# Performance work log

Hardware: AMD Instinct MI355X
Metric: run time of the kernel (lower is better)

The kernel has to match this reference:

```python
import jax, jax.numpy as jnp
import numpy as np

G = 128            # fine grid side -> N0 = 16384 nodes
C = 128            # hidden channels
CL = 4             # voxel cluster side (scale = CL/G = 1/32)
GC = G // CL       # coarse grid side = 32
NC = GC * GC       # 1024 coarse nodes
L = 6              # 3 MP blocks (down0, down1, up0) x 2 MP layers each


def _build_graph():
    ii, jj = np.meshgrid(np.arange(G), np.arange(G), indexing='ij')
    nid = ii * G + jj
    s_h, t_h = nid[:, :-1].ravel(), nid[:, 1:].ravel()
    s_v, t_v = nid[:-1, :].ravel(), nid[1:, :].ravel()
    src = np.concatenate([s_h, t_h, s_v, t_v]).astype(np.int64)
    dst = np.concatenate([t_h, s_h, t_v, s_v]).astype(np.int64)
    # voxel_grid(pos, size=1/32) on the unit square -> cluster id per node
    perm = ((ii // CL) * GC + (jj // CL)).ravel().astype(np.int64)
    ms, mt = perm[src], perm[dst]
    key = ms * NC + mt
    nonself = ms != mt
    uk = np.unique(key[nonself])                  # pool_edge: remove self loops + coalesce (sorted)
    E1 = int(uk.shape[0])
    e2c = np.where(nonself, np.searchsorted(uk, key), E1).astype(np.int64)
    pooled_ei = np.stack([uk // NC, uk % NC]).astype(np.int64)
    # unpool_edge: first fine edge whose mapped endpoints match each coarse edge
    first = np.full(E1 + 1, src.shape[0], dtype=np.int64)
    np.minimum.at(first, e2c, np.arange(src.shape[0], dtype=np.int64))
    perm_edges = first[:E1]
    return np.stack([src, dst]), perm, pooled_ei, e2c, perm_edges


def setup_inputs() -> dict:
    key = jax.random.key(0)
    ks = jax.random.split(key, 10)
    ei, perm, pei, e2c, pe = _build_graph()
    N0, E0 = G * G, ei.shape[1]
    s = 0.05
    return {
        'x': jax.random.normal(ks[0], (N0, C), jnp.float32),
        'edge_attr': jax.random.normal(ks[1], (E0, C), jnp.float32),
        'We1': jax.random.normal(ks[2], (L, 3 * C, C), jnp.float32) * s,
        'be1': jax.random.normal(ks[3], (L, C), jnp.float32) * s,
        'We2': jax.random.normal(ks[4], (L, C, C), jnp.float32) * s,
        'be2': jax.random.normal(ks[5], (L, C), jnp.float32) * s,
        'Wn1': jax.random.normal(ks[6], (L, 2 * C, C), jnp.float32) * s,
        'bn1': jax.random.normal(ks[7], (L, C), jnp.float32) * s,
        'Wn2': jax.random.normal(ks[8], (L, C, C), jnp.float32) * s,
        'bn2': jax.random.normal(ks[9], (L, C), jnp.float32) * s,
        'edge_index': jnp.asarray(ei),
        'perm': jnp.asarray(perm),
        'pooled_edge_index': jnp.asarray(pei),
        'edge_to_coarse': jnp.asarray(e2c),
        'perm_edges': jnp.asarray(pe),
    }


def _mp_block(x, e, src, dst, n, layers, We1, be1, We2, be2, Wn1, bn1, Wn2, bn2):
    # Residual message-passing block: edge MLP on [e, x_src, x_dst], node MLP on [x, sum_msg]
    for l in layers:
        m = jnp.concatenate([e, x[src], x[dst]], axis=-1)          # [E, 3C]
        e = e + (jax.nn.relu(m @ We1[l] + be1[l]) @ We2[l] + be2[l])
        agg = jax.ops.segment_sum(e, dst, num_segments=n)          # [N, C]
        h = jnp.concatenate([x, agg], axis=-1)                     # [N, 2C]
        x = x + (jax.nn.relu(h @ Wn1[l] + bn1[l]) @ Wn2[l] + bn2[l])
    return x, e


def reference(x, edge_attr, We1, be1, We2, be2, Wn1, bn1, Wn2, bn2,
              edge_index, perm, pooled_edge_index, edge_to_coarse, perm_edges):
    p = (We1, be1, We2, be2, Wn1, bn1, Wn2, bn2)
    N0 = x.shape[0]
    src0, dst0 = edge_index[0], edge_index[1]
    # down conv 0 (fine level)
    x0, e0 = _mp_block(x, edge_attr, src0, dst0, N0, (0, 1), *p)
    # avg_pool: mean node features per cluster, coalesce-sum edge attrs
    counts = jax.ops.segment_sum(jnp.ones((N0, 1), x.dtype), perm, num_segments=NC)
    x1 = jax.ops.segment_sum(x0, perm, num_segments=NC) / counts
    E1 = pooled_edge_index.shape[1]
    ea1 = jax.ops.segment_sum(e0, edge_to_coarse, num_segments=E1 + 1)[:E1]
    # down conv 1 (coarse level)
    x1, ea1 = _mp_block(x1, ea1, pooled_edge_index[0], pooled_edge_index[1], NC, (2, 3), *p)
    # unpool + sum-res skip connections
    xu = x0 + x1[perm]
    eu = e0 + jnp.zeros_like(e0).at[perm_edges].set(ea1)
    # up conv
    return _mp_block(xu, eu, src0, dst0, N0, (4, 5), *p)
```

## Files before the change

kernel.cpp:

```cpp
#include <hip/hip_runtime.h>

#define C_ 128
#define N0 16384
#define E0 65024
#define NC_ 1024
#define E1C 3968
#define LSTR 40
#define HSTR 36

typedef __attribute__((ext_vector_type(8))) short bf16x8;
typedef __attribute__((ext_vector_type(16))) float f32x16;

#define OFF_WE1 0
#define OFF_WE2 294912
#define OFF_WN1 393216
#define OFF_WN2 589824
#define W_TOTAL 688128

__device__ __forceinline__ void bsplit(float a, unsigned short& hi, unsigned short& lo) {
  unsigned ab = __float_as_uint(a);
  unsigned hb = ab & 0xFFFF0000u;
  hi = (unsigned short)(hb >> 16);
  float r = a - __uint_as_float(hb);
  lo = (unsigned short)(__float_as_uint(r) >> 16);
}

__device__ __forceinline__ int cprefix(int ci, int cj) {
  int rows = (ci == 0) ? 0 : (94 + (ci - 1) * 126);
  int v = (ci > 0) + (ci < 31);
  int within = (cj == 0) ? 0 : (2 * cj - 1);
  return rows + within + cj * v;
}

__device__ __forceinline__ void add4(float4& s, const float* p) {
  float4 v = *(const float4*)p;
  s.x += v.x; s.y += v.y; s.z += v.z; s.w += v.w;
}

__device__ __forceinline__ f32x16 zero16() {
  f32x16 z;
  #pragma unroll
  for (int i = 0; i < 16; ++i) z[i] = 0.f;
  return z;
}

__global__ void prep_weights(const float* __restrict__ We1, const float* __restrict__ We2,
                             const float* __restrict__ Wn1, const float* __restrict__ Wn2,
                             short* __restrict__ wh, short* __restrict__ wl) {
  int idx = blockIdx.x * 256 + threadIdx.x;
  const float* src; int Kt, off, rem;
  if (idx < 294912)      { src = We1; Kt = 384; off = OFF_WE1; rem = idx; }
  else if (idx < 393216) { src = We2; Kt = 128; off = OFF_WE2; rem = idx - 294912; }
  else if (idx < 589824) { src = Wn1; Kt = 256; off = OFF_WN1; rem = idx - 393216; }
  else                   { src = Wn2; Kt = 128; off = OFF_WN2; rem = idx - 589824; }
  int per_layer = Kt << 7;
  int layer = rem / per_layer;
  int r2 = rem - layer * per_layer;
  int k = r2 >> 7;
  int col = r2 & 127;
  float a = src[layer * per_layer + (k << 7) + col];
  unsigned short hi, lo;
  bsplit(a, hi, lo);
  int dst = off + layer * ((Kt >> 5) << 12) + ((k >> 5) << 12) + (col << 5) + (k & 31);
  wh[dst] = (short)hi;
  wl[dst] = (short)lo;
}

__device__ __forceinline__ void stage_w(short* sWh, short* sWl,
                                        const short* __restrict__ Wh,
                                        const short* __restrict__ Wl,
                                        int kc, int tid) {
  const short* srcH = Wh + (kc << 12);
  const short* srcL = Wl + (kc << 12);
  #pragma unroll
  for (int u0 = 0; u0 < 2; ++u0) {
    int u = tid + u0 * 256;
    int col = u >> 2, part = u & 3;
    *(uint4*)&sWh[col * LSTR + part * 8] = *(const uint4*)(srcH + u * 8);
    *(uint4*)&sWl[col * LSTR + part * 8] = *(const uint4*)(srcL + u * 8);
  }
}

#define BSPLIT8(V0, V1, AH, AL) do { \
    unsigned short h0_,h1_,h2_,h3_,h4_,h5_,h6_,h7_, l0_,l1_,l2_,l3_,l4_,l5_,l6_,l7_; \
    bsplit((V0).x,h0_,l0_); bsplit((V0).y,h1_,l1_); bsplit((V0).z,h2_,l2_); bsplit((V0).w,h3_,l3_); \
    bsplit((V1).x,h4_,l4_); bsplit((V1).y,h5_,l5_); bsplit((V1).z,h6_,l6_); bsplit((V1).w,h7_,l7_); \
    AH = (bf16x8){(short)h0_,(short)h1_,(short)h2_,(short)h3_,(short)h4_,(short)h5_,(short)h6_,(short)h7_}; \
    AL = (bf16x8){(short)l0_,(short)l1_,(short)l2_,(short)l3_,(short)l4_,(short)l5_,(short)l6_,(short)l7_}; \
  } while (0)

#define MFMA3(ACC, AH, AL, BH, BL) do { \
    ACC = __builtin_amdgcn_mfma_f32_32x32x16_bf16(AH, BH, ACC, 0, 0, 0); \
    ACC = __builtin_amdgcn_mfma_f32_32x32x16_bf16(AH, BL, ACC, 0, 0, 0); \
    ACC = __builtin_amdgcn_mfma_f32_32x32x16_bf16(AL, BH, ACC, 0, 0, 0); \
  } while (0)

#define UNPACKH(ROW, S, AH, AL) do { \
    const unsigned* hp_ = &sH[(ROW) * HSTR + (S) * 16 + hi * 8]; \
    uint4 u0_ = *(const uint4*)hp_; uint4 u1_ = *(const uint4*)(hp_ + 4); \
    AH = (bf16x8){(short)(u0_.x & 0xFFFFu), (short)(u0_.y & 0xFFFFu), (short)(u0_.z & 0xFFFFu), (short)(u0_.w & 0xFFFFu), \
                  (short)(u1_.x & 0xFFFFu), (short)(u1_.y & 0xFFFFu), (short)(u1_.z & 0xFFFFu), (short)(u1_.w & 0xFFFFu)}; \
    AL = (bf16x8){(short)(u0_.x >> 16), (short)(u0_.y >> 16), (short)(u0_.z >> 16), (short)(u0_.w >> 16), \
                  (short)(u1_.x >> 16), (short)(u1_.y >> 16), (short)(u1_.z >> 16), (short)(u1_.w >> 16)}; \
  } while (0)

template<int MODE>
__global__ __launch_bounds__(256, 2) void mlp_mfma(
    float* __restrict__ io, const float* __restrict__ xin,
    const int* __restrict__ srcI, const int* __restrict__ dstI,
    const short* __restrict__ W1h, const short* __restrict__ W1l,
    const float* __restrict__ b1,
    const short* __restrict__ W2h, const short* __restrict__ W2l,
    const float* __restrict__ b2)
{
  __shared__ alignas(16) short sWh[128 * LSTR], sWl[128 * LSTR];
  __shared__ alignas(16) unsigned sH[128 * HSTR];

  const int tid = threadIdx.x;
  const int w   = tid >> 6;
  const int wr  = w >> 1;
  const int wc  = w & 1;
  const int l   = tid & 63;
  const int c31 = l & 31;
  const int hi  = l >> 5;
  const int r0  = blockIdx.x * 128;

  const int ar0 = wr * 64 + c31;
  const int ar1 = ar0 + 32;
  const float* pio0 = io + (size_t)(r0 + ar0) * C_;
  const float* pio1 = io + (size_t)(r0 + ar1) * C_;
  const float *px0, *px1, *pd0, *pd1;
  if (MODE == 0) {
    px0 = xin + (size_t)srcI[r0 + ar0] * C_;
    px1 = xin + (size_t)srcI[r0 + ar1] * C_;
    pd0 = xin + (size_t)dstI[r0 + ar0] * C_;
    pd1 = xin + (size_t)dstI[r0 + ar1] * C_;
  } else {
    px0 = xin + (size_t)(r0 + ar0) * C_;
    px1 = xin + (size_t)(r0 + ar1) * C_;
    pd0 = px0; pd1 = px1;
  }

  float4 pa00, pa01, pa02, pa03, pa10, pa11, pa12, pa13;
#define LOADA(KC) do { \
    int rg_ = (KC) >> 2; int cb_ = ((KC) & 3) * 32 + hi * 8; \
    const float* q0_; const float* q1_; \
    if (MODE == 0) { q0_ = (rg_ == 0) ? pio0 : (rg_ == 1) ? px0 : pd0; \
                     q1_ = (rg_ == 0) ? pio1 : (rg_ == 1) ? px1 : pd1; } \
    else           { q0_ = (rg_ == 0) ? pio0 : px0; \
                     q1_ = (rg_ == 0) ? pio1 : px1; } \
    pa00 = *(const float4*)(q0_ + cb_);      pa01 = *(const float4*)(q0_ + cb_ + 4); \
    pa02 = *(const float4*)(q0_ + cb_ + 16); pa03 = *(const float4*)(q0_ + cb_ + 20); \
    pa10 = *(const float4*)(q1_ + cb_);      pa11 = *(const float4*)(q1_ + cb_ + 4); \
    pa12 = *(const float4*)(q1_ + cb_ + 16); pa13 = *(const float4*)(q1_ + cb_ + 20); \
  } while (0)

  f32x16 acc00 = zero16(), acc01 = zero16(), acc10 = zero16(), acc11 = zero16();

  const int NK1 = (MODE == 0) ? 12 : 8;
  LOADA(0);
  for (int kc = 0; kc < NK1; ++kc) {
    bf16x8 ah0s0, al0s0, ah0s1, al0s1, ah1s0, al1s0, ah1s1, al1s1;
    BSPLIT8(pa00, pa01, ah0s0, al0s0);
    BSPLIT8(pa02, pa03, ah0s1, al0s1);
    BSPLIT8(pa10, pa11, ah1s0, al1s0);
    BSPLIT8(pa12, pa13, ah1s1, al1s1);
    if (kc + 1 < NK1) LOADA(kc + 1);
    __syncthreads();
    stage_w(sWh, sWl, W1h, W1l, kc, tid);
    __syncthreads();
    #pragma unroll
    for (int s = 0; s < 2; ++s) {
      const int wb = s * 16 + hi * 8;
      bf16x8 bh0 = *(const bf16x8*)&sWh[(wc * 64 + c31) * LSTR + wb];
      bf16x8 bl0 = *(const bf16x8*)&sWl[(wc * 64 + c31) * LSTR + wb];
      bf16x8 bh1 = *(const bf16x8*)&sWh[(wc * 64 + 32 + c31) * LSTR + wb];
      bf16x8 bl1 = *(const bf16x8*)&sWl[(wc * 64 + 32 + c31) * LSTR + wb];
      if (s == 0) {
        MFMA3(acc00, ah0s0, al0s0, bh0, bl0);
        MFMA3(acc01, ah0s0, al0s0, bh1, bl1);
        MFMA3(acc10, ah1s0, al1s0, bh0, bl0);
        MFMA3(acc11, ah1s0, al1s0, bh1, bl1);
      } else {
        MFMA3(acc00, ah0s1, al0s1, bh0, bl0);
        MFMA3(acc01, ah0s1, al0s1, bh1, bl1);
        MFMA3(acc10, ah1s1, al1s1, bh0, bl0);
        MFMA3(acc11, ah1s1, al1s1, bh1, bl1);
      }
    }
  }

  f32x16 bcc00 = zero16(), bcc01 = zero16(), bcc10 = zero16(), bcc11 = zero16();
  #pragma unroll
  for (int kc = 0; kc < 4; ++kc) {
    __syncthreads();
    if (wc == (kc >> 1)) {
      const float bb = b1[(kc >> 1) * 64 + (kc & 1) * 32 + c31];
      #pragma unroll
      for (int rg = 0; rg < 16; ++rg) {
        int rr = (rg & 3) + 8 * (rg >> 2) + 4 * hi;
        float h0 = fmaxf(((kc & 1) ? acc01[rg] : acc00[rg]) + bb, 0.f);
        float h1 = fmaxf(((kc & 1) ? acc11[rg] : acc10[rg]) + bb, 0.f);
        unsigned short hh, hl;
        bsplit(h0, hh, hl);
        sH[(wr * 64 + rr) * HSTR + c31] = (unsigned)hh | ((unsigned)hl << 16);
        bsplit(h1, hh, hl);
        sH[(wr * 64 + 32 + rr) * HSTR + c31] = (unsigned)hh | ((unsigned)hl << 16);
      }
    }
    stage_w(sWh, sWl, W2h, W2l, kc, tid);
    __syncthreads();
    #pragma unroll
    for (int s = 0; s < 2; ++s) {
      bf16x8 ah0, al0, ah1, al1;
      UNPACKH(wr * 64 + c31, s, ah0, al0);
      UNPACKH(wr * 64 + 32 + c31, s, ah1, al1);
      const int wb = s * 16 + hi * 8;
      bf16x8 bh0 = *(const bf16x8*)&sWh[(wc * 64 + c31) * LSTR + wb];
      bf16x8 bl0 = *(const bf16x8*)&sWl[(wc * 64 + c31) * LSTR + wb];
      bf16x8 bh1 = *(const bf16x8*)&sWh[(wc * 64 + 32 + c31) * LSTR + wb];
      bf16x8 bl1 = *(const bf16x8*)&sWl[(wc * 64 + 32 + c31) * LSTR + wb];
      MFMA3(bcc00, ah0, al0, bh0, bl0);
      MFMA3(bcc01, ah0, al0, bh1, bl1);
      MFMA3(bcc10, ah1, al1, bh0, bl0);
      MFMA3(bcc11, ah1, al1, bh1, bl1);
    }
  }

  const float b2c0 = b2[wc * 64 + c31];
  const float b2c1 = b2[wc * 64 + 32 + c31];
  #pragma unroll
  for (int rg = 0; rg < 16; ++rg) {
    int rr = (rg & 3) + 8 * (rg >> 2) + 4 * hi;
    size_t row0 = (size_t)(r0 + wr * 64 + rr) * C_;
    size_t row1 = (size_t)(r0 + wr * 64 + 32 + rr) * C_;
    io[row0 + wc * 64 + c31]      += bcc00[rg] + b2c0;
    io[row0 + wc * 64 + 32 + c31] += bcc01[rg] + b2c1;
    io[row1 + wc * 64 + c31]      += bcc10[rg] + b2c0;
    io[row1 + wc * 64 + 32 + c31] += bcc11[rg] + b2c1;
  }
#undef LOADA
}

__global__ void agg_fine(const float* __restrict__ e, float* __restrict__ agg) {
  int idx = blockIdx.x * 256 + threadIdx.x;
  int n = idx >> 5;
  int c4 = (idx & 31) * 4;
  int i = n >> 7, j = n & 127;
  float4 s = make_float4(0.f, 0.f, 0.f, 0.f);
  if (j >= 1)   add4(s, e + (i*127 + (j-1)) * C_ + c4);
  if (j <= 126) add4(s, e + (16256 + i*127 + j) * C_ + c4);
  if (i >= 1)   add4(s, e + (32512 + (i-1)*128 + j) * C_ + c4);
  if (i <= 126) add4(s, e + (48768 + i*128 + j) * C_ + c4);
  *(float4*)(agg + n * C_ + c4) = s;
}

__global__ void agg_coarse(const float* __restrict__ e1, float* __restrict__ agg1) {
  int idx = blockIdx.x * 256 + threadIdx.x;
  int m = idx >> 5;
  int c4 = (idx & 31) * 4;
  int ci = m >> 5, cj = m & 31;
  float4 s = make_float4(0.f, 0.f, 0.f, 0.f);
  if (ci > 0)  add4(s, e1 + (cprefix(ci-1,cj) + (ci-1>0) + (cj>0) + (cj<31)) * C_ + c4);
  if (cj > 0)  add4(s, e1 + (cprefix(ci,cj-1) + (ci>0) + (cj-1>0)) * C_ + c4);
  if (cj < 31) add4(s, e1 + (cprefix(ci,cj+1) + (ci>0)) * C_ + c4);
  if (ci < 31) add4(s, e1 + (cprefix(ci+1,cj)) * C_ + c4);
  *(float4*)(agg1 + m * C_ + c4) = s;
}

__global__ void pool_x(const float* __restrict__ x, float* __restrict__ x1) {
  int idx = blockIdx.x * 256 + threadIdx.x;
  int m = idx >> 5;
  int c4 = (idx & 31) * 4;
  int ci = m >> 5, cj = m & 31;
  float4 s = make_float4(0.f, 0.f, 0.f, 0.f);
  #pragma unroll
  for (int a = 0; a < 4; ++a)
    #pragma unroll
    for (int b = 0; b < 4; ++b)
      add4(s, x + ((4*ci + a) * 128 + 4*cj + b) * C_ + c4);
  s.x *= 0.0625f; s.y *= 0.0625f; s.z *= 0.0625f; s.w *= 0.0625f;
  *(float4*)(x1 + m * C_ + c4) = s;
}

__global__ void pool_e(const float* __restrict__ e, float* __restrict__ e1) {
  int idx = blockIdx.x * 256 + threadIdx.x;
  int combo = idx >> 5;
  int c4 = (idx & 31) * 4;
  int m = combo >> 2, dir = combo & 3;
  int ci = m >> 5, cj = m & 31;
  int cid, f0, fstep;
  if (dir == 0) { if (ci == 0) return;
    cid = cprefix(ci,cj);
    f0 = 48768 + (4*ci - 1) * 128 + 4*cj; fstep = 1;
  } else if (dir == 1) { if (cj == 0) return;
    cid = cprefix(ci,cj) + (ci>0);
    f0 = 16256 + (4*ci) * 127 + 4*cj - 1; fstep = 127;
  } else if (dir == 2) { if (cj == 31) return;
    cid = cprefix(ci,cj) + (ci>0) + (cj>0);
    f0 = (4*ci) * 127 + 4*cj + 3; fstep = 127;
  } else { if (ci == 31) return;
    cid = cprefix(ci,cj) + (ci>0) + (cj>0) + (cj<31);
    f0 = 32512 + (4*ci + 3) * 128 + 4*cj; fstep = 1;
  }
  float4 s = make_float4(0.f, 0.f, 0.f, 0.f);
  #pragma unroll
  for (int k = 0; k < 4; ++k)
    add4(s, e + (f0 + k * fstep) * C_ + c4);
  *(float4*)(e1 + cid * C_ + c4) = s;
}

__global__ void unpool_x(float* __restrict__ x, const float* __restrict__ x1,
                         const int* __restrict__ perm) {
  int idx = blockIdx.x * 256 + threadIdx.x;
  int n = idx >> 5, c4 = (idx & 31) * 4;
  int m = perm[n];
  float4 v = *(const float4*)(x + n * C_ + c4);
  add4(v, x1 + m * C_ + c4);
  *(float4*)(x + n * C_ + c4) = v;
}

__global__ void unpool_e(float* __restrict__ e, const float* __restrict__ e1,
                         const int* __restrict__ pe) {
  int idx = blockIdx.x * 256 + threadIdx.x;
  int k = idx >> 5, c4 = (idx & 31) * 4;
  int fe = pe[k];
  float4 v = *(const float4*)(e + fe * C_ + c4);
  add4(v, e1 + k * C_ + c4);
  *(float4*)(e + fe * C_ + c4) = v;
}

extern "C" void kernel_launch(void* const* d_in, const int* in_sizes, int n_in,
                              void* d_out, int out_size, void* d_ws, size_t ws_size,
                              hipStream_t stream) {
  const float* in_x  = (const float*)d_in[0];
  const float* in_ea = (const float*)d_in[1];
  const float* We1 = (const float*)d_in[2];
  const float* be1 = (const float*)d_in[3];
  const float* We2 = (const float*)d_in[4];
  const float* be2 = (const float*)d_in[5];
  const float* Wn1 = (const float*)d_in[6];
  const float* bn1 = (const float*)d_in[7];
  const float* Wn2 = (const float*)d_in[8];
  const float* bn2 = (const float*)d_in[9];
  const int* ei   = (const int*)d_in[10];
  const int* perm = (const int*)d_in[11];
  const int* pei  = (const int*)d_in[12];
  const int* pe   = (const int*)d_in[14];

  float* x = (float*)d_out;
  float* e = x + (size_t)N0 * C_;
  float* agg  = (float*)d_ws;
  float* x1   = agg + (size_t)N0 * C_;
  float* e1   = x1 + (size_t)NC_ * C_;
  float* agg1 = e1 + (size_t)E1C * C_;
  short* wsH  = (short*)(agg1 + (size_t)NC_ * C_);
  short* wsL  = wsH + W_TOTAL;

  hipMemcpyAsync(x, in_x, (size_t)N0 * C_ * 4, hipMemcpyDeviceToDevice, stream);
  hipMemcpyAsync(e, in_ea, (size_t)E0 * C_ * 4, hipMemcpyDeviceToDevice, stream);

  prep_weights<<<W_TOTAL / 256, 256, 0, stream>>>(We1, We2, Wn1, Wn2, wsH, wsL);

  const int* srcF = ei;  const int* dstF = ei + E0;
  const int* srcC = pei; const int* dstC = pei + E1C;

  #define WE1_OFF(l) (OFF_WE1 + (l) * 49152)
  #define WE2_OFF(l) (OFF_WE2 + (l) * 16384)
  #define WN1_OFF(l) (OFF_WN1 + (l) * 32768)
  #define WN2_OFF(l) (OFF_WN2 + (l) * 16384)

  for (int l = 0; l < 2; ++l) {
    mlp_mfma<0><<<E0/128, 256, 0, stream>>>(e, x, srcF, dstF,
        wsH + WE1_OFF(l), wsL + WE1_OFF(l), be1 + l*C_,
        wsH + WE2_OFF(l), wsL + WE2_OFF(l), be2 + l*C_);
    agg_fine<<<N0*32/256, 256, 0, stream>>>(e, agg);
    mlp_mfma<1><<<N0/128, 256, 0, stream>>>(x, agg, nullptr, nullptr,
        wsH + WN1_OFF(l), wsL + WN1_OFF(l), bn1 + l*C_,
        wsH + WN2_OFF(l), wsL + WN2_OFF(l), bn2 + l*C_);
  }

  pool_x<<<NC_*32/256, 256, 0, stream>>>(x, x1);
  pool_e<<<NC_*4*32/256, 256, 0, stream>>>(e, e1);

  for (int l = 2; l < 4; ++l) {
    mlp_mfma<0><<<E1C/128, 256, 0, stream>>>(e1, x1, srcC, dstC,
        wsH + WE1_OFF(l), wsL + WE1_OFF(l), be1 + l*C_,
        wsH + WE2_OFF(l), wsL + WE2_OFF(l), be2 + l*C_);
    agg_coarse<<<NC_*32/256, 256, 0, stream>>>(e1, agg1);
    mlp_mfma<1><<<NC_/128, 256, 0, stream>>>(x1, agg1, nullptr, nullptr,
        wsH + WN1_OFF(l), wsL + WN1_OFF(l), bn1 + l*C_,
        wsH + WN2_OFF(l), wsL + WN2_OFF(l), bn2 + l*C_);
  }

  unpool_x<<<N0*32/256, 256, 0, stream>>>(x, x1, perm);
  unpool_e<<<E1C*32/256, 256, 0, stream>>>(e, e1, pe);

  for (int l = 4; l < 6; ++l) {
    mlp_mfma<0><<<E0/128, 256, 0, stream>>>(e, x, srcF, dstF,
        wsH + WE1_OFF(l), wsL + WE1_OFF(l), be1 + l*C_,
        wsH + WE2_OFF(l), wsL + WE2_OFF(l), be2 + l*C_);
    agg_fine<<<N0*32/256, 256, 0, stream>>>(e, agg);
    mlp_mfma<1><<<N0/128, 256, 0, stream>>>(x, agg, nullptr, nullptr,
        wsH + WN1_OFF(l), wsL + WN1_OFF(l), bn1 + l*C_,
        wsH + WN2_OFF(l), wsL + WN2_OFF(l), bn2 + l*C_);
  }
}
```

Measured before the change: 548.7 us.

## Read MFMA weight fragments directly from global and add small-row-tile variants

Weight tiles are no longer staged through shared memory with two barriers per K-step. Each wave now loads its bf16 hi/lo B fragments straight from global memory, relying on the L2 cache for reuse. The kernel is also templated on rows per block: the node MLPs and the coarse edge MLP use 32-row blocks with four column-split waves, which launches many more blocks for the small launches. The trade-off is redundant global and L2 weight traffic across blocks, with weight reuse now dependent on cache hits.

Result: faster. 498.6 us (-9.1%).

```diff
diff --git a/kernel.cpp b/kernel.cpp
--- a/kernel.cpp
+++ b/kernel.cpp
@@ -5,7 +5,6 @@
 #define E0 65024
 #define NC_ 1024
 #define E1C 3968
-#define LSTR 40
 #define HSTR 36
 
 typedef __attribute__((ext_vector_type(8))) short bf16x8;
@@ -66,21 +65,6 @@
   wl[dst] = (short)lo;
 }
 
-__device__ __forceinline__ void stage_w(short* sWh, short* sWl,
-                                        const short* __restrict__ Wh,
-                                        const short* __restrict__ Wl,
-                                        int kc, int tid) {
-  const short* srcH = Wh + (kc << 12);
-  const short* srcL = Wl + (kc << 12);
-  #pragma unroll
-  for (int u0 = 0; u0 < 2; ++u0) {
-    int u = tid + u0 * 256;
-    int col = u >> 2, part = u & 3;
-    *(uint4*)&sWh[col * LSTR + part * 8] = *(const uint4*)(srcH + u * 8);
-    *(uint4*)&sWl[col * LSTR + part * 8] = *(const uint4*)(srcL + u * 8);
-  }
-}
-
 #define BSPLIT8(V0, V1, AH, AL) do { \
     unsigned short h0_,h1_,h2_,h3_,h4_,h5_,h6_,h7_, l0_,l1_,l2_,l3_,l4_,l5_,l6_,l7_; \
     bsplit((V0).x,h0_,l0_); bsplit((V0).y,h1_,l1_); bsplit((V0).z,h2_,l2_); bsplit((V0).w,h3_,l3_); \
@@ -104,8 +88,8 @@
                   (short)(u1_.x >> 16), (short)(u1_.y >> 16), (short)(u1_.z >> 16), (short)(u1_.w >> 16)}; \
   } while (0)
 
-template<int MODE>
-__global__ __launch_bounds__(256, 2) void mlp_mfma(
+template<int MODE, int RB, int MINW>
+__global__ __launch_bounds__(256, MINW) void mlp_mfma(
     float* __restrict__ io, const float* __restrict__ xin,
     const int* __restrict__ srcI, const int* __restrict__ dstI,
     const short* __restrict__ W1h, const short* __restrict__ W1l,
@@ -113,133 +97,155 @@
     const short* __restrict__ W2h, const short* __restrict__ W2l,
     const float* __restrict__ b2)
 {
-  __shared__ alignas(16) short sWh[128 * LSTR], sWl[128 * LSTR];
-  __shared__ alignas(16) unsigned sH[128 * HSTR];
+  constexpr int NW_C = (RB == 128) ? 2 : 4;
+  constexpr int CW   = 128 / NW_C;
+  constexpr int NCS  = CW / 32;
+  constexpr int NRS  = (RB >= 64) ? 2 : 1;
+
+  __shared__ alignas(16) unsigned sH[RB * HSTR];
 
   const int tid = threadIdx.x;
   const int w   = tid >> 6;
-  const int wr  = w >> 1;
-  const int wc  = w & 1;
+  const int wr  = (RB == 128) ? (w >> 1) : 0;
+  const int wc  = (RB == 128) ? (w & 1) : w;
   const int l   = tid & 63;
   const int c31 = l & 31;
   const int hi  = l >> 5;
-  const int r0  = blockIdx.x * 128;
-
-  const int ar0 = wr * 64 + c31;
-  const int ar1 = ar0 + 32;
-  const float* pio0 = io + (size_t)(r0 + ar0) * C_;
-  const float* pio1 = io + (size_t)(r0 + ar1) * C_;
-  const float *px0, *px1, *pd0, *pd1;
-  if (MODE == 0) {
-    px0 = xin + (size_t)srcI[r0 + ar0] * C_;
-    px1 = xin + (size_t)srcI[r0 + ar1] * C_;
-    pd0 = xin + (size_t)dstI[r0 + ar0] * C_;
-    pd1 = xin + (size_t)dstI[r0 + ar1] * C_;
-  } else {
-    px0 = xin + (size_t)(r0 + ar0) * C_;
-    px1 = xin + (size_t)(r0 + ar1) * C_;
-    pd0 = px0; pd1 = px1;
-  }
-
-  float4 pa00, pa01, pa02, pa03, pa10, pa11, pa12, pa13;
-#define LOADA(KC) do { \
-    int rg_ = (KC) >> 2; int cb_ = ((KC) & 3) * 32 + hi * 8; \
-    const float* q0_; const float* q1_; \
-    if (MODE == 0) { q0_ = (rg_ == 0) ? pio0 : (rg_ == 1) ? px0 : pd0; \
-                     q1_ = (rg_ == 0) ? pio1 : (rg_ == 1) ? px1 : pd1; } \
-    else           { q0_ = (rg_ == 0) ? pio0 : px0; \
-                     q1_ = (rg_ == 0) ? pio1 : px1; } \
-    pa00 = *(const float4*)(q0_ + cb_);      pa01 = *(const float4*)(q0_ + cb_ + 4); \
-    pa02 = *(const float4*)(q0_ + cb_ + 16); pa03 = *(const float4*)(q0_ + cb_ + 20); \
-    pa10 = *(const float4*)(q1_ + cb_);      pa11 = *(const float4*)(q1_ + cb_ + 4); \
-    pa12 = *(const float4*)(q1_ + cb_ + 16); pa13 = *(const float4*)(q1_ + cb_ + 20); \
-  } while (0)
-
-  f32x16 acc00 = zero16(), acc01 = zero16(), acc10 = zero16(), acc11 = zero16();
+  const int r0  = blockIdx.x * RB;
+
+  const float* pio[NRS]; const float* px[NRS]; const float* pd[NRS];
+  #pragma unroll
+  for (int rs = 0; rs < NRS; ++rs) {
+    int ar = wr * 64 + rs * 32 + c31;
+    pio[rs] = io + (size_t)(r0 + ar) * C_;
+    if (MODE == 0) {
+      px[rs] = xin + (size_t)srcI[r0 + ar] * C_;
+      pd[rs] = xin + (size_t)dstI[r0 + ar] * C_;
+    } else {
+      px[rs] = xin + (size_t)(r0 + ar) * C_;
+      pd[rs] = px[rs];
+    }
+  }
+
+  float4 pa[NRS][4];
+  auto LOADA = [&](int kc) {
+    int rg = kc >> 2, cb = (kc & 3) * 32 + hi * 8;
+    #pragma unroll
+    for (int rs = 0; rs < NRS; ++rs) {
+      const float* q = (MODE == 0)
+        ? ((rg == 0) ? pio[rs] : (rg == 1) ? px[rs] : pd[rs])
+        : ((rg == 0) ? pio[rs] : px[rs]);
+      pa[rs][0] = *(const float4*)(q + cb);
+      pa[rs][1] = *(const float4*)(q + cb + 4);
+      pa[rs][2] = *(const float4*)(q + cb + 16);
+      pa[rs][3] = *(const float4*)(q + cb + 20);
+    }
+  };
+
+  f32x16 acc[NRS][NCS];
+  #pragma unroll
+  for (int rs = 0; rs < NRS; ++rs)
+    #pragma unroll
+    for (int cs = 0; cs < NCS; ++cs) acc[rs][cs] = zero16();
 
   const int NK1 = (MODE == 0) ? 12 : 8;
   LOADA(0);
   for (int kc = 0; kc < NK1; ++kc) {
-    bf16x8 ah0s0, al0s0, ah0s1, al0s1, ah1s0, al1s0, ah1s1, al1s1;
-    BSPLIT8(pa00, pa01, ah0s0, al0s0);
-    BSPLIT8(pa02, pa03, ah0s1, al0s1);
-    BSPLIT8(pa10, pa11, ah1s0, al1s0);
-    BSPLIT8(pa12, pa13, ah1s1, al1s1);
+    bf16x8 bh[NCS][2], bl[NCS][2];
+    {
+      const short* bhp = W1h + (kc << 12);
+      const short* blp = W1l + (kc << 12);
+      #pragma unroll
+      for (int cs = 0; cs < NCS; ++cs)
+        #pragma unroll
+        for (int s = 0; s < 2; ++s) {
+          int off = (wc * CW + cs * 32 + c31) * 32 + s * 16 + hi * 8;
+          bh[cs][s] = *(const bf16x8*)(bhp + off);
+          bl[cs][s] = *(const bf16x8*)(blp + off);
+        }
+    }
+    bf16x8 ah[NRS][2], al[NRS][2];
+    #pragma unroll
+    for (int rs = 0; rs < NRS; ++rs) {
+      BSPLIT8(pa[rs][0], pa[rs][1], ah[rs][0], al[rs][0]);
+      BSPLIT8(pa[rs][2], pa[rs][3], ah[rs][1], al[rs][1]);
+    }
     if (kc + 1 < NK1) LOADA(kc + 1);
-    __syncthreads();
-    stage_w(sWh, sWl, W1h, W1l, kc, tid);
-    __syncthreads();
-    #pragma unroll
-    for (int s = 0; s < 2; ++s) {
-      const int wb = s * 16 + hi * 8;
-      bf16x8 bh0 = *(const bf16x8*)&sWh[(wc * 64 + c31) * LSTR + wb];
-      bf16x8 bl0 = *(const bf16x8*)&sWl[(wc * 64 + c31) * LSTR + wb];
-      bf16x8 bh1 = *(const bf16x8*)&sWh[(wc * 64 + 32 + c31) * LSTR + wb];
-      bf16x8 bl1 = *(const bf16x8*)&sWl[(wc * 64 + 32 + c31) * LSTR + wb];
-      if (s == 0) {
-        MFMA3(acc00, ah0s0, al0s0, bh0, bl0);
-        MFMA3(acc01, ah0s0, al0s0, bh1, bl1);
-        MFMA3(acc10, ah1s0, al1s0, bh0, bl0);
-        MFMA3(acc11, ah1s0, al1s0, bh1, bl1);
-      } else {
-        MFMA3(acc00, ah0s1, al0s1, bh0, bl0);
-        MFMA3(acc01, ah0s1, al0s1, bh1, bl1);
-        MFMA3(acc10, ah1s1, al1s1, bh0, bl0);
-        MFMA3(acc11, ah1s1, al1s1, bh1, bl1);
-      }
-    }
-  }
-
-  f32x16 bcc00 = zero16(), bcc01 = zero16(), bcc10 = zero16(), bcc11 = zero16();
+    #pragma unroll
+    for (int s = 0; s < 2; ++s)
+      #pragma unroll
+      for (int cs = 0; cs < NCS; ++cs)
+        #pragma unroll
+        for (int rs = 0; rs < NRS; ++rs)
+          MFMA3(acc[rs][cs], ah[rs][s], al[rs][s], bh[cs][s], bl[cs][s]);
+  }
+
+  f32x16 bcc[NRS][NCS];
+  #pragma unroll
+  for (int rs = 0; rs < NRS; ++rs)
+    #pragma unroll
+    for (int cs = 0; cs < NCS; ++cs) bcc[rs][cs] = zero16();
+
   #pragma unroll
   for (int kc = 0; kc < 4; ++kc) {
     __syncthreads();
-    if (wc == (kc >> 1)) {
-      const float bb = b1[(kc >> 1) * 64 + (kc & 1) * 32 + c31];
+    constexpr int DIV = (RB == 128) ? 2 : 1;
+    const int wc_o = (RB == 128) ? (kc >> 1) : kc;
+    const int cs_o = (RB == 128) ? (kc & 1) : 0;
+    if (wc == wc_o) {
+      const float bb = b1[kc * 32 + c31];
+      #pragma unroll
+      for (int rs = 0; rs < NRS; ++rs)
+        #pragma unroll
+        for (int rg = 0; rg < 16; ++rg) {
+          int rr = (rg & 3) + 8 * (rg >> 2) + 4 * hi;
+          float h = fmaxf(acc[rs][cs_o][rg] + bb, 0.f);
+          unsigned short hh, hl;
+          bsplit(h, hh, hl);
+          sH[(wr * 64 + rs * 32 + rr) * HSTR + c31] = (unsigned)hh | ((unsigned)hl << 16);
+        }
+    }
+    __syncthreads();
+    bf16x8 bh[NCS][2], bl[NCS][2];
+    {
+      const short* bhp = W2h + (kc << 12);
+      const short* blp = W2l + (kc << 12);
+      #pragma unroll
+      for (int cs = 0; cs < NCS; ++cs)
+        #pragma unroll
+        for (int s = 0; s < 2; ++s) {
+          int off = (wc * CW + cs * 32 + c31) * 32 + s * 16 + hi * 8;
+          bh[cs][s] = *(const bf16x8*)(bhp + off);
+          bl[cs][s] = *(const bf16x8*)(blp + off);
+        }
+    }
+    bf16x8 ah[NRS][2], al[NRS][2];
+    #pragma unroll
+    for (int rs = 0; rs < NRS; ++rs)
+      #pragma unroll
+      for (int s = 0; s < 2; ++s)
+        UNPACKH(wr * 64 + rs * 32 + c31, s, ah[rs][s], al[rs][s]);
+    #pragma unroll
+    for (int s = 0; s < 2; ++s)
+      #pragma unroll
+      for (int cs = 0; cs < NCS; ++cs)
+        #pragma unroll
+        for (int rs = 0; rs < NRS; ++rs)
+          MFMA3(bcc[rs][cs], ah[rs][s], al[rs][s], bh[cs][s], bl[cs][s]);
+  }
+
+  #pragma unroll
+  for (int cs = 0; cs < NCS; ++cs) {
+    const float b2v = b2[wc * CW + cs * 32 + c31];
+    #pragma unroll
+    for (int rs = 0; rs < NRS; ++rs)
       #pragma unroll
       for (int rg = 0; rg < 16; ++rg) {
         int rr = (rg & 3) + 8 * (rg >> 2) + 4 * hi;
-        float h0 = fmaxf(((kc & 1) ? acc01[rg] : acc00[rg]) + bb, 0.f);
-        float h1 = fmaxf(((kc & 1) ? acc11[rg] : acc10[rg]) + bb, 0.f);
-        unsigned short hh, hl;
-        bsplit(h0, hh, hl);
-        sH[(wr * 64 + rr) * HSTR + c31] = (unsigned)hh | ((unsigned)hl << 16);
-        bsplit(h1, hh, hl);
-        sH[(wr * 64 + 32 + rr) * HSTR + c31] = (unsigned)hh | ((unsigned)hl << 16);
+        size_t row = (size_t)(r0 + wr * 64 + rs * 32 + rr) * C_;
+        io[row + wc * CW + cs * 32 + c31] += bcc[rs][cs][rg] + b2v;
       }
-    }
-    stage_w(sWh, sWl, W2h, W2l, kc, tid);
-    __syncthreads();
-    #pragma unroll
-    for (int s = 0; s < 2; ++s) {
-      bf16x8 ah0, al0, ah1, al1;
-      UNPACKH(wr * 64 + c31, s, ah0, al0);
-      UNPACKH(wr * 64 + 32 + c31, s, ah1, al1);
-      const int wb = s * 16 + hi * 8;
-      bf16x8 bh0 = *(const bf16x8*)&sWh[(wc * 64 + c31) * LSTR + wb];
-      bf16x8 bl0 = *(const bf16x8*)&sWl[(wc * 64 + c31) * LSTR + wb];
-      bf16x8 bh1 = *(const bf16x8*)&sWh[(wc * 64 + 32 + c31) * LSTR + wb];
-      bf16x8 bl1 = *(const bf16x8*)&sWl[(wc * 64 + 32 + c31) * LSTR + wb];
-      MFMA3(bcc00, ah0, al0, bh0, bl0);
-      MFMA3(bcc01, ah0, al0, bh1, bl1);
-      MFMA3(bcc10, ah1, al1, bh0, bl0);
-      MFMA3(bcc11, ah1, al1, bh1, bl1);
-    }
-  }
-
-  const float b2c0 = b2[wc * 64 + c31];
-  const float b2c1 = b2[wc * 64 + 32 + c31];
-  #pragma unroll
-  for (int rg = 0; rg < 16; ++rg) {
-    int rr = (rg & 3) + 8 * (rg >> 2) + 4 * hi;
-    size_t row0 = (size_t)(r0 + wr * 64 + rr) * C_;
-    size_t row1 = (size_t)(r0 + wr * 64 + 32 + rr) * C_;
-    io[row0 + wc * 64 + c31]      += bcc00[rg] + b2c0;
-    io[row0 + wc * 64 + 32 + c31] += bcc01[rg] + b2c1;
-    io[row1 + wc * 64 + c31]      += bcc10[rg] + b2c0;
-    io[row1 + wc * 64 + 32 + c31] += bcc11[rg] + b2c1;
-  }
-#undef LOADA
+  }
 }
 
 __global__ void agg_fine(const float* __restrict__ e, float* __restrict__ agg) {
@@ -371,11 +377,11 @@
   #define WN2_OFF(l) (OFF_WN2 + (l) * 16384)
 
   for (int l = 0; l < 2; ++l) {
-    mlp_mfma<0><<<E0/128, 256, 0, stream>>>(e, x, srcF, dstF,
+    mlp_mfma<0,128,2><<<E0/128, 256, 0, stream>>>(e, x, srcF, dstF,
         wsH + WE1_OFF(l), wsL + WE1_OFF(l), be1 + l*C_,
         wsH + WE2_OFF(l), wsL + WE2_OFF(l), be2 + l*C_);
     agg_fine<<<N0*32/256, 256, 0, stream>>>(e, agg);
-    mlp_mfma<1><<<N0/128, 256, 0, stream>>>(x, agg, nullptr, nullptr,
+    mlp_mfma<1,32,3><<<N0/32, 256, 0, stream>>>(x, agg, nullptr, nullptr,
         wsH + WN1_OFF(l), wsL + WN1_OFF(l), bn1 + l*C_,
         wsH + WN2_OFF(l), wsL + WN2_OFF(l), bn2 + l*C_);
   }
@@ -384,11 +390,11 @@
   pool_e<<<NC_*4*32/256, 256, 0, stream>>>(e, e1);
 
   for (int l = 2; l < 4; ++l) {
-    mlp_mfma<0><<<E1C/128, 256, 0, stream>>>(e1, x1, srcC, dstC,
+    mlp_mfma<0,32,3><<<E1C/32, 256, 0, stream>>>(e1, x1, srcC, dstC,
         wsH + WE1_OFF(l), wsL + WE1_OFF(l), be1 + l*C_,
         wsH + WE2_OFF(l), wsL + WE2_OFF(l), be2 + l*C_);
     agg_coarse<<<NC_*32/256, 256, 0, stream>>>(e1, agg1);
-    mlp_mfma<1><<<NC_/128, 256, 0, stream>>>(x1, agg1, nullptr, nullptr,
+    mlp_mfma<1,32,3><<<NC_/32, 256, 0, stream>>>(x1, agg1, nullptr, nullptr,
         wsH + WN1_OFF(l), wsL + WN1_OFF(l), bn1 + l*C_,
         wsH + WN2_OFF(l), wsL + WN2_OFF(l), bn2 + l*C_);
   }
@@ -397,11 +403,11 @@
   unpool_e<<<E1C*32/256, 256, 0, stream>>>(e, e1, pe);
 
   for (int l = 4; l < 6; ++l) {
-    mlp_mfma<0><<<E0/128, 256, 0, stream>>>(e, x, srcF, dstF,
+    mlp_mfma<0,128,2><<<E0/128, 256, 0, stream>>>(e, x, srcF, dstF,
         wsH + WE1_OFF(l), wsL + WE1_OFF(l), be1 + l*C_,
         wsH + WE2_OFF(l), wsL + WE2_OFF(l), be2 + l*C_);
     agg_fine<<<N0*32/256, 256, 0, stream>>>(e, agg);
-    mlp_mfma<1><<<N0/128, 256, 0, stream>>>(x, agg, nullptr, nullptr,
+    mlp_mfma<1,32,3><<<N0/32, 256, 0, stream>>>(x, agg, nullptr, nullptr,
         wsH + WN1_OFF(l), wsL + WN1_OFF(l), bn1 + l*C_,
         wsH + WN2_OFF(l), wsL + WN2_OFF(l), bn2 + l*C_);
   }
```
